# Optimization experiments

Hardware: AMD Instinct MI355X
Metric: run time of the kernel (lower is better)

Reference implementation:

```python
import jax, jax.numpy as jnp
import numpy as np

B, N, L = 256, 4096, 6
EMBED, HID, VOCAB = 16, 32, 200
NOTE, LSTM_D, T = 64, 64, 128


def _tree_structure():
    """One random tree of N nodes (root=node 0), tiled across the batch.
    height = distance above deepest descendant; children have strictly smaller height."""
    rng = np.random.default_rng(0)
    height = np.zeros(N, np.int32)
    height[0] = L
    height[1:] = rng.integers(0, L, N - 1)
    kind = np.full(N, 2, np.int32)  # 2 = internal
    leaf_mask = height == 0
    kind[leaf_mask] = (rng.random(leaf_mask.sum()) < 0.1).astype(np.int32)  # 1=ptr, 0=leaf
    parent = np.zeros(N, np.int64)
    for hl in range(L):
        mask = height == hl
        cand = np.where((height > hl) & (kind == 2))[0]  # root always qualifies
        parent[mask] = rng.choice(cand, size=int(mask.sum()))
    parent[0] = 0  # root points to itself; harmless (its own h stays 0 until final level)
    return height, kind, parent


def setup_inputs():
    height, kind, parent = _tree_structure()
    offs = (np.arange(B, dtype=np.int64) * N)[:, None]
    rng = np.random.default_rng(1)
    inp = {
        'kind': jnp.asarray(np.tile(kind, B), jnp.int32),
        'height': jnp.asarray(np.tile(height, B), jnp.int32),
        'parent': jnp.asarray((parent[None, :] + offs).reshape(-1), jnp.int32),
        'tok_a': jnp.asarray(rng.integers(0, VOCAB, B * N), jnp.int32),
        'tok_b': jnp.asarray(rng.integers(0, VOCAB, B * N), jnp.int32),
        'ptr_time': jnp.asarray(rng.integers(0, T, B * N), jnp.int32),
    }
    key = jax.random.key(0)
    ks = jax.random.split(key, 16)
    def w(k, shape, scale=0.05):
        return (jax.random.normal(k, shape, jnp.float32) * scale)
    inp['first_notes'] = w(ks[0], (B, NOTE), 1.0)
    inp['lstm_out'] = w(ks[1], (B, T, LSTM_D), 1.0)
    inp['embedding'] = w(ks[2], (VOCAB, EMBED), 0.02)
    inp['leaf_w1'] = w(ks[3], (2 * EMBED, HID)); inp['leaf_b1'] = w(ks[4], (HID,))
    inp['leaf_w2'] = w(ks[5], (HID, HID));       inp['leaf_b2'] = w(ks[6], (HID,))
    inp['node_w'] = w(ks[7], (2 * EMBED + HID, HID)); inp['node_b'] = w(ks[8], (HID,))
    inp['ptr_w'] = w(ks[9], (NOTE + LSTM_D, HID));    inp['ptr_b'] = w(ks[10], (HID,))
    inp['ff_w1'] = w(ks[11], (HID, HID)); inp['ff_b1'] = w(ks[12], (HID,))
    inp['ff_w2'] = w(ks[13], (HID, HID)); inp['ff_b2'] = w(ks[14], (HID,))
    inp['tail_w'] = w(ks[15], (HID, 1)); inp['tail_b'] = jnp.zeros((1,), jnp.float32)
    return inp


def reference(kind, height, parent, tok_a, tok_b, ptr_time, first_notes, lstm_out,
              embedding, leaf_w1, leaf_b1, leaf_w2, leaf_b2, node_w, node_b,
              ptr_w, ptr_b, ff_w1, ff_b1, ff_w2, ff_b2, tail_w, tail_b):
    M = kind.shape[0]
    nb = first_notes.shape[0]
    n_per = M // nb
    tree_id = jnp.arange(M, dtype=jnp.int32) // n_per
    emb_a = embedding[tok_a]  # [M, EMBED] (parent-type / first-token embed)
    emb_b = embedding[tok_b]  # [M, EMBED] (node-type / second-token embed)
    pair = jnp.concatenate([emb_a, emb_b], axis=-1)  # [M, 2*EMBED]
    # leaf path: two stacked linears (no nonlinearity), as in leaf_ff
    leaf_h = (pair @ leaf_w1 + leaf_b1) @ leaf_w2 + leaf_b2
    # ptr path: Linear(note_dim + lstm_out_dim -> hidden)
    ptr_in = jnp.concatenate([first_notes[tree_id], lstm_out[tree_id, ptr_time]], axis=-1)
    ptr_h = ptr_in @ ptr_w + ptr_b
    h = jnp.where((kind == 0)[:, None], leaf_h,
                  jnp.where((kind == 1)[:, None], ptr_h, 0.0))
    # level-synchronous child-sum: children always have smaller height
    for lvl in range(1, L + 1):
        csum = jax.ops.segment_sum(h, parent, num_segments=M)  # [M, HID]
        inner = jax.nn.relu(jnp.concatenate([pair, csum], axis=-1) @ node_w + node_b)
        h = jnp.where((height == lvl)[:, None], inner, h)
    roots = h[::n_per]  # [B, HID], root is node 0 of each tree block
    ff = (roots @ ff_w1 + ff_b1) @ ff_w2 + ff_b2
    return ff @ tail_w + tail_b  # [B, 1]


if __name__ == '__main__':
    out = reference(**setup_inputs())
    print(out.shape, out.dtype)
```

## Files before the change

### kernel.cpp

```cpp
#include <hip/hip_runtime.h>

#define BATCH   256
#define N_PER   4096
#define EMBED   16
#define HID     32
#define NOTE    64
#define LSTM_D  64
#define T_LEN   128
#define VOCAB   200
#define HSTR    (BATCH * HID)

#define MH_C0    0
#define MH_C1    1
#define MH_CNT   2
#define MH_P     7
#define MH_PBASE 8
#define OFF_K0N   64
#define OFF_K0S   (OFF_K0N + N_PER)
#define OFF_K1N   (OFF_K0S + N_PER)
#define OFF_K1S   (OFF_K1N + N_PER)
#define OFF_PLIST (OFF_K1S + N_PER)
#define OFF_WSLOT (OFF_PLIST + N_PER)
#define OFF_COFF  (OFF_WSLOT + N_PER)
#define EAW_OFF     (1024 * 1024)
#define EBW_OFF     (EAW_OFF + VOCAB * HID * 4)
#define FN_PRE_OFF  (1536 * 1024)
#define ROOTSUM_OFF (1792 * 1024)
#define PTRPRE_OFF  (2ull * 1024 * 1024)
#define H_OFF       (8ull * 1024 * 1024)

#define RCHUNK 16

__global__ __launch_bounds__(1024) void build_structure(
    const int* __restrict__ kind, const int* __restrict__ height,
    const int* __restrict__ parent, int* __restrict__ meta)
{
    __shared__ unsigned long long p64[1024];
    __shared__ int pint[1024];
    __shared__ int node2pidx[N_PER];
    __shared__ int deg[N_PER];
    __shared__ int sbases[8];
    __shared__ int stot[8];

    int t  = threadIdx.x;
    int i0 = 4 * t;

    int myb[4];
    #pragma unroll
    for (int q = 0; q < 4; ++q) {
        int i = i0 + q;
        int hgt = height[i];
        int b;
        if (hgt > 0) { b = 1 + hgt; if (b > 7) b = 7; }
        else b = (kind[i] == 0) ? 0 : 1;
        myb[q] = b;
    }
    unsigned long long clo = 0, chi = 0;
    #pragma unroll
    for (int q = 0; q < 4; ++q) {
        int b = myb[q];
        if (b < 4) clo += 1ull << (16 * b);
        else       chi += 1ull << (16 * (b - 4));
    }
    p64[t] = clo; __syncthreads();
    for (int off = 1; off < 1024; off <<= 1) {
        unsigned long long v = (t >= off) ? p64[t - off] : 0ull; __syncthreads();
        p64[t] += v; __syncthreads();
    }
    unsigned long long inc_lo = p64[t];
    if (t == 1023) {
        stot[0] = (int)(inc_lo & 0xFFFF);         stot[1] = (int)((inc_lo >> 16) & 0xFFFF);
        stot[2] = (int)((inc_lo >> 32) & 0xFFFF); stot[3] = (int)((inc_lo >> 48) & 0xFFFF);
    }
    __syncthreads();
    p64[t] = chi; __syncthreads();
    for (int off = 1; off < 1024; off <<= 1) {
        unsigned long long v = (t >= off) ? p64[t - off] : 0ull; __syncthreads();
        p64[t] += v; __syncthreads();
    }
    unsigned long long inc_hi = p64[t];
    if (t == 1023) {
        stot[4] = (int)(inc_hi & 0xFFFF);         stot[5] = (int)((inc_hi >> 16) & 0xFFFF);
        stot[6] = (int)((inc_hi >> 32) & 0xFFFF); stot[7] = (int)((inc_hi >> 48) & 0xFFFF);
    }
    __syncthreads();
    if (t == 0) {
        int s = 0;
        for (int b = 0; b < 8; ++b) { sbases[b] = s; s += stot[b]; }
        meta[MH_C0] = stot[0];
        meta[MH_C1] = stot[1];
        for (int l = 0; l < 5; ++l) meta[MH_CNT + l]   = stot[2 + l];
        for (int l = 0; l < 5; ++l) meta[MH_PBASE + l] = sbases[2 + l] - sbases[2];
        meta[MH_P] = (sbases[7] - sbases[2]) + stot[7];
    }
    __syncthreads();

    unsigned long long exlo = inc_lo - clo, exhi = inc_hi - chi;
    int mypos[4], mypidx[4];
    #pragma unroll
    for (int q = 0; q < 4; ++q) {
        int i = i0 + q, b = myb[q];
        int pos;
        if (b < 4) { pos = (int)((exlo >> (16 * b)) & 0xFFFF); exlo += 1ull << (16 * b); }
        else       { pos = (int)((exhi >> (16 * (b - 4))) & 0xFFFF); exhi += 1ull << (16 * (b - 4)); }
        mypos[q] = pos;
        int pidx = -1;
        if (b == 0)      meta[OFF_K0N + pos] = i;
        else if (b == 1) meta[OFF_K1N + pos] = i;
        else {
            pidx = (sbases[b] - sbases[2]) + pos;
            meta[OFF_PLIST + pidx] = i;
            node2pidx[i] = pidx;
        }
        mypidx[q] = pidx;
    }
    #pragma unroll
    for (int q = 0; q < 4; ++q) deg[i0 + q] = 0;
    __syncthreads();

    int par[4];
    #pragma unroll
    for (int q = 0; q < 4; ++q) {
        int i = i0 + q; par[q] = parent[i];
        if (i != 0) atomicAdd(&deg[node2pidx[par[q]]], 1);
    }
    __syncthreads();

    int d0 = deg[i0], d1 = deg[i0 + 1], d2 = deg[i0 + 2], d3 = deg[i0 + 3];
    int s4 = d0 + d1 + d2 + d3;
    pint[t] = s4; __syncthreads();
    for (int off = 1; off < 1024; off <<= 1) {
        int v = (t >= off) ? pint[t - off] : 0; __syncthreads();
        pint[t] += v; __syncthreads();
    }
    int ex = pint[t] - s4;
    int o0 = ex, o1 = ex + d0, o2 = o1 + d1, o3 = o2 + d2;
    deg[i0] = o0; deg[i0 + 1] = o1; deg[i0 + 2] = o2; deg[i0 + 3] = o3;
    meta[OFF_COFF + i0]     = o0;
    meta[OFF_COFF + i0 + 1] = o1;
    meta[OFF_COFF + i0 + 2] = o2;
    meta[OFF_COFF + i0 + 3] = o3;
    if (t == 1023) meta[OFF_COFF + N_PER] = o3 + d3;
    __syncthreads();

    #pragma unroll
    for (int q = 0; q < 4; ++q) {
        int i = i0 + q; if (i == 0) continue;
        int slot = atomicAdd(&deg[node2pidx[par[q]]], 1);
        int b = myb[q];
        if (b == 0)      meta[OFF_K0S + mypos[q]] = slot;
        else if (b == 1) meta[OFF_K1S + mypos[q]] = slot;
        else             meta[OFF_WSLOT + mypidx[q]] = slot;
    }
}

__global__ __launch_bounds__(256) void prep_kernel(
    const int* __restrict__ meta,
    const int* __restrict__ tok_a, const int* __restrict__ tok_b,
    const float* __restrict__ first_notes, const float* __restrict__ lstm_out,
    const float* __restrict__ embedding,
    const float* __restrict__ leaf_w1, const float* __restrict__ leaf_b1,
    const float* __restrict__ leaf_w2, const float* __restrict__ leaf_b2,
    const float* __restrict__ node_w,
    const float* __restrict__ ptr_w, const float* __restrict__ ptr_b,
    float* __restrict__ eaw_g, float* __restrict__ ebw_g,
    float* __restrict__ fn_pre, float* __restrict__ ptr_pre,
    float* __restrict__ h)
{
    int tid  = blockIdx.x * blockDim.x + threadIdx.x;
    int nthr = gridDim.x * blockDim.x;
    int lane = threadIdx.x & 31;
    int gid  = tid >> 5;
    int ngr  = nthr >> 5;

    for (int idx = tid; idx < VOCAB * HID; idx += nthr) {
        int v = idx >> 5, d = idx & 31;
        float sa = 0.f, sb = 0.f;
        #pragma unroll
        for (int k = 0; k < EMBED; ++k) {
            float e = embedding[v * EMBED + k];
            sa += e * node_w[k * HID + d];
            sb += e * node_w[(EMBED + k) * HID + d];
        }
        eaw_g[idx] = sa;
        ebw_g[idx] = sb;
    }

    for (int r = gid; r < BATCH; r += ngr) {
        const float* fn = first_notes + (size_t)r * NOTE;
        float v = ptr_b[lane];
        #pragma unroll
        for (int k = 0; k < NOTE; ++k) v += fn[k] * ptr_w[k * HID + lane];
        fn_pre[r * HID + lane] = v;
    }

    for (int r = gid; r < BATCH * T_LEN; r += ngr) {
        const float* lo = lstm_out + (size_t)r * LSTM_D;
        float v = 0.f;
        #pragma unroll
        for (int k = 0; k < LSTM_D; ++k) v += lo[k] * ptr_w[(NOTE + k) * HID + lane];
        ptr_pre[r * HID + lane] = v;
    }

    {
        int c0 = meta[MH_C0];
        const int* K0N = meta + OFF_K0N;
        const int* K0S = meta + OFF_K0S;
        float w1a[EMBED], w1b[EMBED], w2c[HID];
        #pragma unroll
        for (int k = 0; k < EMBED; ++k) {
            w1a[k] = leaf_w1[k * HID + lane];
            w1b[k] = leaf_w1[(EMBED + k) * HID + lane];
        }
        #pragma unroll
        for (int k = 0; k < HID; ++k) w2c[k] = leaf_w2[k * HID + lane];
        float b1 = leaf_b1[lane], b2 = leaf_b2[lane];

        int tot = c0 * BATCH;
        for (int i = gid; i < tot; i += ngr) {
            int j = i >> 8, tree = i & 255;
            int node = K0N[j], slot = K0S[j];
            int gn = tree * N_PER + node;
            const float* ea = embedding + tok_a[gn] * EMBED;
            const float* eb = embedding + tok_b[gn] * EMBED;
            float hid = b1;
            #pragma unroll
            for (int k = 0; k < EMBED; ++k) hid += ea[k] * w1a[k];
            #pragma unroll
            for (int k = 0; k < EMBED; ++k) hid += eb[k] * w1b[k];
            float v = b2;
            #pragma unroll
            for (int k = 0; k < HID; ++k) v += __shfl(hid, k, 32) * w2c[k];
            h[(size_t)slot * HSTR + tree * HID + lane] = v;
        }
    }
}

__global__ __launch_bounds__(256) void ptr_kernel(
    const int* __restrict__ meta, const int* __restrict__ ptr_time,
    const float* __restrict__ fn_pre, const float* __restrict__ ptr_pre,
    float* __restrict__ h)
{
    int c1 = meta[MH_C1];
    const int* K1N = meta + OFF_K1N;
    const int* K1S = meta + OFF_K1S;
    int lane = threadIdx.x & 31;
    int gid  = (blockIdx.x * blockDim.x + threadIdx.x) >> 5;
    int ngr  = (gridDim.x * blockDim.x) >> 5;

    int tot = c1 * BATCH;
    for (int i = gid; i < tot; i += ngr) {
        int j = i >> 8, tree = i & 255;
        int node = K1N[j], slot = K1S[j];
        int tt = ptr_time[tree * N_PER + node];
        float v = fn_pre[tree * HID + lane]
                + ptr_pre[((size_t)tree * T_LEN + tt) * HID + lane];
        h[(size_t)slot * HSTR + tree * HID + lane] = v;
    }
}

__global__ __launch_bounds__(256) void level_kernel(
    const int* __restrict__ meta,
    const int* __restrict__ tok_a, const int* __restrict__ tok_b,
    const float* __restrict__ eaw_g, const float* __restrict__ ebw_g,
    const float* __restrict__ node_w, const float* __restrict__ node_b,
    float* __restrict__ h, int lvl)
{
    int cnt = meta[MH_CNT + lvl];
    int pb  = meta[MH_PBASE + lvl];
    const int* PL = meta + OFF_PLIST;
    const int* WS = meta + OFF_WSLOT;
    const int* CO = meta + OFF_COFF;

    int lane = threadIdx.x & 31;
    int gid  = (blockIdx.x * blockDim.x + threadIdx.x) >> 5;
    int ngr  = (gridDim.x * blockDim.x) >> 5;

    float wc[HID];
    #pragma unroll
    for (int k = 0; k < HID; ++k) wc[k] = node_w[(2 * EMBED + k) * HID + lane];
    float nb = node_b[lane];

    int perchunk = cnt << 5;
    int tot = cnt * BATCH;
    for (int i = gid; i < tot; i += ngr) {
        int tchunk = i / perchunk;
        int r      = i - tchunk * perchunk;
        int rr     = r >> 5;
        int tree   = (tchunk << 5) + (r & 31);
        int pidx = pb + rr;
        int node = PL[pidx], wslot = WS[pidx];
        int e = CO[pidx], e1 = CO[pidx + 1];

        const float* hb = h + (size_t)tree * HID + lane;
        float csum = 0.f;
        for (int c = e; c < e1; ++c) csum += hb[(size_t)c * HSTR];

        int gn = tree * N_PER + node;
        int ta = tok_a[gn], tb = tok_b[gn];
        float v = nb + eaw_g[ta * HID + lane] + ebw_g[tb * HID + lane];
        #pragma unroll
        for (int k = 0; k < HID; ++k) v += __shfl(csum, k, 32) * wc[k];
        v = fmaxf(v, 0.f);
        h[(size_t)wslot * HSTR + tree * HID + lane] = v;
    }
}

__global__ __launch_bounds__(256) void root_gather_kernel(
    const int* __restrict__ meta, const float* __restrict__ h,
    float* __restrict__ rootsum)
{
    const int* CO = meta + OFF_COFF;
    int P = meta[MH_P];
    int e = CO[P - 1], e1 = CO[P];
    int n = e1 - e;
    int per = (n + RCHUNK - 1) / RCHUNK;

    int t = blockIdx.x * blockDim.x + threadIdx.x;
    int lane  = t & 31;
    int tree  = (t >> 5) & 255;
    int chunk = t >> 13;
    if (chunk >= RCHUNK) return;

    int s  = e + chunk * per;
    int en = s + per; if (en > e1) en = e1;
    if (s >= en) return;
    float sum = 0.f;
    for (int c = s; c < en; ++c)
        sum += h[(size_t)c * HSTR + tree * HID + lane];
    atomicAdd(&rootsum[tree * HID + lane], sum);
}

__global__ __launch_bounds__(256) void final_kernel(
    const int* __restrict__ meta,
    const int* __restrict__ tok_a, const int* __restrict__ tok_b,
    const float* __restrict__ eaw_g, const float* __restrict__ ebw_g,
    const float* __restrict__ rootsum,
    const float* __restrict__ node_w, const float* __restrict__ node_b,
    const float* __restrict__ ff_w1, const float* __restrict__ ff_b1,
    const float* __restrict__ ff_w2, const float* __restrict__ ff_b2,
    const float* __restrict__ tail_w, const float* __restrict__ tail_b,
    float* __restrict__ out)
{
    int tree = (blockIdx.x * blockDim.x + threadIdx.x) >> 5;
    int lane = threadIdx.x & 31;
    if (tree >= BATCH) return;

    float csum = rootsum[tree * HID + lane];
    int gn = tree * N_PER;
    int ta = tok_a[gn], tb = tok_b[gn];
    float v = node_b[lane] + eaw_g[ta * HID + lane] + ebw_g[tb * HID + lane];
    #pragma unroll
    for (int k = 0; k < HID; ++k)
        v += __shfl(csum, k, 32) * node_w[(2 * EMBED + k) * HID + lane];
    v = fmaxf(v, 0.f);

    float f1 = ff_b1[lane];
    #pragma unroll
    for (int k = 0; k < HID; ++k) f1 += __shfl(v, k, 32) * ff_w1[k * HID + lane];
    float f2 = ff_b2[lane];
    #pragma unroll
    for (int k = 0; k < HID; ++k) f2 += __shfl(f1, k, 32) * ff_w2[k * HID + lane];

    float c2 = f2 * tail_w[lane];
    #pragma unroll
    for (int off = 16; off > 0; off >>= 1) c2 += __shfl_down(c2, off, 32);
    if (lane == 0) out[tree] = c2 + tail_b[0];
}

extern "C" void kernel_launch(void* const* d_in, const int* in_sizes, int n_in,
                              void* d_out, int out_size, void* d_ws, size_t ws_size,
                              hipStream_t stream) {
    const int*   kind        = (const int*)d_in[0];
    const int*   height      = (const int*)d_in[1];
    const int*   parent      = (const int*)d_in[2];
    const int*   tok_a       = (const int*)d_in[3];
    const int*   tok_b       = (const int*)d_in[4];
    const int*   ptr_time    = (const int*)d_in[5];
    const float* first_notes = (const float*)d_in[6];
    const float* lstm_out    = (const float*)d_in[7];
    const float* embedding   = (const float*)d_in[8];
    const float* leaf_w1     = (const float*)d_in[9];
    const float* leaf_b1     = (const float*)d_in[10];
    const float* leaf_w2     = (const float*)d_in[11];
    const float* leaf_b2     = (const float*)d_in[12];
    const float* node_w      = (const float*)d_in[13];
    const float* node_b      = (const float*)d_in[14];
    const float* ptr_w       = (const float*)d_in[15];
    const float* ptr_b       = (const float*)d_in[16];
    const float* ff_w1       = (const float*)d_in[17];
    const float* ff_b1       = (const float*)d_in[18];
    const float* ff_w2       = (const float*)d_in[19];
    const float* ff_b2       = (const float*)d_in[20];
    const float* tail_w      = (const float*)d_in[21];
    const float* tail_b      = (const float*)d_in[22];

    char* ws = (char*)d_ws;
    int*   meta    = (int*)ws;
    float* eaw_g   = (float*)(ws + EAW_OFF);
    float* ebw_g   = (float*)(ws + EBW_OFF);
    float* fn_pre  = (float*)(ws + FN_PRE_OFF);
    float* rootsum = (float*)(ws + ROOTSUM_OFF);
    float* ptr_pre = (float*)(ws + PTRPRE_OFF);
    float* h       = (float*)(ws + H_OFF);

    hipMemsetAsync(rootsum, 0, BATCH * HID * sizeof(float), stream);

    build_structure<<<1, 1024, 0, stream>>>(kind, height, parent, meta);

    prep_kernel<<<2048, 256, 0, stream>>>(
        meta, tok_a, tok_b, first_notes, lstm_out, embedding,
        leaf_w1, leaf_b1, leaf_w2, leaf_b2, node_w, ptr_w, ptr_b,
        eaw_g, ebw_g, fn_pre, ptr_pre, h);

    ptr_kernel<<<2048, 256, 0, stream>>>(meta, ptr_time, fn_pre, ptr_pre, h);

    for (int lvl = 0; lvl < 5; ++lvl) {
        level_kernel<<<4096, 256, 0, stream>>>(
            meta, tok_a, tok_b, eaw_g, ebw_g, node_w, node_b, h, lvl);
    }

    root_gather_kernel<<<(RCHUNK * BATCH * HID) / 256, 256, 0, stream>>>(
        meta, h, rootsum);

    final_kernel<<<32, 256, 0, stream>>>(
        meta, tok_a, tok_b, eaw_g, ebw_g, rootsum, node_w, node_b,
        ff_w1, ff_b1, ff_w2, ff_b2, tail_w, tail_b, (float*)d_out);
}
```

Before: 399.6 us.

## Fold leaf MLP into vocab tables, compute ptr rows on demand, use wave scans

The structure builder now uses wavefront shuffle scans instead of block-wide shared-memory scans. It also precomputes per-vocab leaf tables (embedding·W1·W2) and the node_w embedding projections, so leaf nodes become two table lookups plus a constant. The ptr path no longer precomputes projections for all B·T lstm rows; it computes only the needed ptr nodes directly, which removes the separate ptr kernel and a large intermediate buffer. The level kernel child-sum is unrolled four ways with independent accumulators. The trade-offs are a redundant ptr_w dot product per ptr node and extra serial work in the single-block build kernel.

Result: slower. 433.6 us (+8.5%).

```diff
diff --git a/kernel.cpp b/kernel.cpp
--- a/kernel.cpp
+++ b/kernel.cpp
@@ -24,19 +24,34 @@
 #define OFF_COFF  (OFF_WSLOT + N_PER)
 #define EAW_OFF     (1024 * 1024)
 #define EBW_OFF     (EAW_OFF + VOCAB * HID * 4)
-#define FN_PRE_OFF  (1536 * 1024)
+#define LA2_OFF     (EBW_OFF + VOCAB * HID * 4)
+#define LB2_OFF     (LA2_OFF + VOCAB * HID * 4)
+#define CC_OFF      (LB2_OFF + VOCAB * HID * 4)
 #define ROOTSUM_OFF (1792 * 1024)
-#define PTRPRE_OFF  (2ull * 1024 * 1024)
 #define H_OFF       (8ull * 1024 * 1024)
 
 #define RCHUNK 16
+
+__device__ __forceinline__ unsigned long long shflup64(unsigned long long x, int off) {
+    unsigned lo = (unsigned)(x & 0xffffffffull);
+    unsigned hi = (unsigned)(x >> 32);
+    lo = __shfl_up(lo, off, 64);
+    hi = __shfl_up(hi, off, 64);
+    return ((unsigned long long)hi << 32) | (unsigned long long)lo;
+}
 
 __global__ __launch_bounds__(1024) void build_structure(
     const int* __restrict__ kind, const int* __restrict__ height,
-    const int* __restrict__ parent, int* __restrict__ meta)
+    const int* __restrict__ parent, int* __restrict__ meta,
+    const float* __restrict__ embedding,
+    const float* __restrict__ leaf_w1, const float* __restrict__ leaf_b1,
+    const float* __restrict__ leaf_w2, const float* __restrict__ leaf_b2,
+    const float* __restrict__ node_w,
+    float* __restrict__ eaw_g, float* __restrict__ ebw_g,
+    float* __restrict__ la2, float* __restrict__ lb2, float* __restrict__ cc)
 {
-    __shared__ unsigned long long p64[1024];
-    __shared__ int pint[1024];
+    __shared__ unsigned long long wlo[16], whi[16];
+    __shared__ int wint[16];
     __shared__ int node2pidx[N_PER];
     __shared__ int deg[N_PER];
     __shared__ int sbases[8];
@@ -44,6 +59,8 @@
 
     int t  = threadIdx.x;
     int i0 = 4 * t;
+    int laneid = t & 63;
+    int wid    = t >> 6;
 
     int myb[4];
     #pragma unroll
@@ -62,31 +79,28 @@
         if (b < 4) clo += 1ull << (16 * b);
         else       chi += 1ull << (16 * (b - 4));
     }
-    p64[t] = clo; __syncthreads();
-    for (int off = 1; off < 1024; off <<= 1) {
-        unsigned long long v = (t >= off) ? p64[t - off] : 0ull; __syncthreads();
-        p64[t] += v; __syncthreads();
-    }
-    unsigned long long inc_lo = p64[t];
-    if (t == 1023) {
-        stot[0] = (int)(inc_lo & 0xFFFF);         stot[1] = (int)((inc_lo >> 16) & 0xFFFF);
-        stot[2] = (int)((inc_lo >> 32) & 0xFFFF); stot[3] = (int)((inc_lo >> 48) & 0xFFFF);
-    }
-    __syncthreads();
-    p64[t] = chi; __syncthreads();
-    for (int off = 1; off < 1024; off <<= 1) {
-        unsigned long long v = (t >= off) ? p64[t - off] : 0ull; __syncthreads();
-        p64[t] += v; __syncthreads();
-    }
-    unsigned long long inc_hi = p64[t];
-    if (t == 1023) {
-        stot[4] = (int)(inc_hi & 0xFFFF);         stot[5] = (int)((inc_hi >> 16) & 0xFFFF);
-        stot[6] = (int)((inc_hi >> 32) & 0xFFFF); stot[7] = (int)((inc_hi >> 48) & 0xFFFF);
-    }
-    __syncthreads();
+
+    unsigned long long a = clo, b64 = chi;
+    #pragma unroll
+    for (int off = 1; off < 64; off <<= 1) {
+        unsigned long long ua = shflup64(a, off);
+        unsigned long long ub = shflup64(b64, off);
+        if (laneid >= off) { a += ua; b64 += ub; }
+    }
+    if (laneid == 63) { wlo[wid] = a; whi[wid] = b64; }
+    __syncthreads();
+    unsigned long long blo = 0, bhi = 0;
+    for (int w = 0; w < wid; ++w) { blo += wlo[w]; bhi += whi[w]; }
+    unsigned long long inc_lo = a + blo, inc_hi = b64 + bhi;
     if (t == 0) {
+        unsigned long long tlo = 0, thi = 0;
+        for (int w = 0; w < 16; ++w) { tlo += wlo[w]; thi += whi[w]; }
+        stot[0] = (int)(tlo & 0xFFFF);         stot[1] = (int)((tlo >> 16) & 0xFFFF);
+        stot[2] = (int)((tlo >> 32) & 0xFFFF); stot[3] = (int)((tlo >> 48) & 0xFFFF);
+        stot[4] = (int)(thi & 0xFFFF);         stot[5] = (int)((thi >> 16) & 0xFFFF);
+        stot[6] = (int)((thi >> 32) & 0xFFFF); stot[7] = (int)((thi >> 48) & 0xFFFF);
         int s = 0;
-        for (int b = 0; b < 8; ++b) { sbases[b] = s; s += stot[b]; }
+        for (int bb = 0; bb < 8; ++bb) { sbases[bb] = s; s += stot[bb]; }
         meta[MH_C0] = stot[0];
         meta[MH_C1] = stot[1];
         for (int l = 0; l < 5; ++l) meta[MH_CNT + l]   = stot[2 + l];
@@ -128,12 +142,20 @@
 
     int d0 = deg[i0], d1 = deg[i0 + 1], d2 = deg[i0 + 2], d3 = deg[i0 + 3];
     int s4 = d0 + d1 + d2 + d3;
-    pint[t] = s4; __syncthreads();
-    for (int off = 1; off < 1024; off <<= 1) {
-        int v = (t >= off) ? pint[t - off] : 0; __syncthreads();
-        pint[t] += v; __syncthreads();
-    }
-    int ex = pint[t] - s4;
+
+    int vi = s4;
+    #pragma unroll
+    for (int off = 1; off < 64; off <<= 1) {
+        int u = __shfl_up(vi, off, 64);
+        if (laneid >= off) vi += u;
+    }
+    if (laneid == 63) wint[wid] = vi;
+    __syncthreads();
+    int bint = 0;
+    for (int w = 0; w < wid; ++w) bint += wint[w];
+    int incl = vi + bint;
+
+    int ex = incl - s4;
     int o0 = ex, o1 = ex + d0, o2 = o1 + d1, o3 = o2 + d2;
     deg[i0] = o0; deg[i0 + 1] = o1; deg[i0 + 2] = o2; deg[i0 + 3] = o3;
     meta[OFF_COFF + i0]     = o0;
@@ -152,19 +174,49 @@
         else if (b == 1) meta[OFF_K1S + mypos[q]] = slot;
         else             meta[OFF_WSLOT + mypidx[q]] = slot;
     }
+
+    {
+        int hw = t >> 5, ln = t & 31;
+        for (int v = hw; v < VOCAB; v += 32) {
+            const float* ev = embedding + v * EMBED;
+            float ea = 0.f, eb = 0.f, t1a = 0.f, t1b = 0.f;
+            #pragma unroll
+            for (int k = 0; k < EMBED; ++k) {
+                float e = ev[k];
+                ea  += e * node_w[k * HID + ln];
+                eb  += e * node_w[(EMBED + k) * HID + ln];
+                t1a += e * leaf_w1[k * HID + ln];
+                t1b += e * leaf_w1[(EMBED + k) * HID + ln];
+            }
+            eaw_g[v * HID + ln] = ea;
+            ebw_g[v * HID + ln] = eb;
+            float a2 = 0.f, b2v = 0.f;
+            #pragma unroll
+            for (int k = 0; k < HID; ++k) {
+                float w2 = leaf_w2[k * HID + ln];
+                a2  += __shfl(t1a, k, 32) * w2;
+                b2v += __shfl(t1b, k, 32) * w2;
+            }
+            la2[v * HID + ln] = a2;
+            lb2[v * HID + ln] = b2v;
+        }
+        if (t < HID) {
+            float c = leaf_b2[t];
+            #pragma unroll
+            for (int k = 0; k < HID; ++k) c += leaf_b1[k] * leaf_w2[k * HID + t];
+            cc[t] = c;
+        }
+    }
 }
 
 __global__ __launch_bounds__(256) void prep_kernel(
     const int* __restrict__ meta,
     const int* __restrict__ tok_a, const int* __restrict__ tok_b,
+    const int* __restrict__ ptr_time,
     const float* __restrict__ first_notes, const float* __restrict__ lstm_out,
-    const float* __restrict__ embedding,
-    const float* __restrict__ leaf_w1, const float* __restrict__ leaf_b1,
-    const float* __restrict__ leaf_w2, const float* __restrict__ leaf_b2,
-    const float* __restrict__ node_w,
+    const float* __restrict__ la2, const float* __restrict__ lb2,
+    const float* __restrict__ cc,
     const float* __restrict__ ptr_w, const float* __restrict__ ptr_b,
-    float* __restrict__ eaw_g, float* __restrict__ ebw_g,
-    float* __restrict__ fn_pre, float* __restrict__ ptr_pre,
     float* __restrict__ h)
 {
     int tid  = blockIdx.x * blockDim.x + threadIdx.x;
@@ -173,89 +225,42 @@
     int gid  = tid >> 5;
     int ngr  = nthr >> 5;
 
-    for (int idx = tid; idx < VOCAB * HID; idx += nthr) {
-        int v = idx >> 5, d = idx & 31;
-        float sa = 0.f, sb = 0.f;
-        #pragma unroll
-        for (int k = 0; k < EMBED; ++k) {
-            float e = embedding[v * EMBED + k];
-            sa += e * node_w[k * HID + d];
-            sb += e * node_w[(EMBED + k) * HID + d];
-        }
-        eaw_g[idx] = sa;
-        ebw_g[idx] = sb;
-    }
-
-    for (int r = gid; r < BATCH; r += ngr) {
-        const float* fn = first_notes + (size_t)r * NOTE;
-        float v = ptr_b[lane];
-        #pragma unroll
-        for (int k = 0; k < NOTE; ++k) v += fn[k] * ptr_w[k * HID + lane];
-        fn_pre[r * HID + lane] = v;
-    }
-
-    for (int r = gid; r < BATCH * T_LEN; r += ngr) {
-        const float* lo = lstm_out + (size_t)r * LSTM_D;
-        float v = 0.f;
-        #pragma unroll
-        for (int k = 0; k < LSTM_D; ++k) v += lo[k] * ptr_w[(NOTE + k) * HID + lane];
-        ptr_pre[r * HID + lane] = v;
-    }
-
     {
+        float ccv = cc[lane];
         int c0 = meta[MH_C0];
         const int* K0N = meta + OFF_K0N;
         const int* K0S = meta + OFF_K0S;
-        float w1a[EMBED], w1b[EMBED], w2c[HID];
-        #pragma unroll
-        for (int k = 0; k < EMBED; ++k) {
-            w1a[k] = leaf_w1[k * HID + lane];
-            w1b[k] = leaf_w1[(EMBED + k) * HID + lane];
-        }
-        #pragma unroll
-        for (int k = 0; k < HID; ++k) w2c[k] = leaf_w2[k * HID + lane];
-        float b1 = leaf_b1[lane], b2 = leaf_b2[lane];
-
         int tot = c0 * BATCH;
         for (int i = gid; i < tot; i += ngr) {
             int j = i >> 8, tree = i & 255;
             int node = K0N[j], slot = K0S[j];
             int gn = tree * N_PER + node;
-            const float* ea = embedding + tok_a[gn] * EMBED;
-            const float* eb = embedding + tok_b[gn] * EMBED;
-            float hid = b1;
+            int ta = tok_a[gn], tb = tok_b[gn];
+            h[(size_t)slot * HSTR + tree * HID + lane] =
+                ccv + la2[ta * HID + lane] + lb2[tb * HID + lane];
+        }
+    }
+
+    {
+        float pb = ptr_b[lane];
+        int c1 = meta[MH_C1];
+        const int* K1N = meta + OFF_K1N;
+        const int* K1S = meta + OFF_K1S;
+        int tot = c1 * BATCH;
+        for (int i = gid; i < tot; i += ngr) {
+            int j = i >> 8, tree = i & 255;
+            int node = K1N[j], slot = K1S[j];
+            int gn = tree * N_PER + node;
+            int tt = ptr_time[gn];
+            const float* fn = first_notes + (size_t)tree * NOTE;
+            const float* lo = lstm_out + ((size_t)tree * T_LEN + tt) * LSTM_D;
+            float v = pb;
             #pragma unroll
-            for (int k = 0; k < EMBED; ++k) hid += ea[k] * w1a[k];
+            for (int k = 0; k < NOTE; ++k)   v += fn[k] * ptr_w[k * HID + lane];
             #pragma unroll
-            for (int k = 0; k < EMBED; ++k) hid += eb[k] * w1b[k];
-            float v = b2;
-            #pragma unroll
-            for (int k = 0; k < HID; ++k) v += __shfl(hid, k, 32) * w2c[k];
+            for (int k = 0; k < LSTM_D; ++k) v += lo[k] * ptr_w[(NOTE + k) * HID + lane];
             h[(size_t)slot * HSTR + tree * HID + lane] = v;
         }
-    }
-}
-
-__global__ __launch_bounds__(256) void ptr_kernel(
-    const int* __restrict__ meta, const int* __restrict__ ptr_time,
-    const float* __restrict__ fn_pre, const float* __restrict__ ptr_pre,
-    float* __restrict__ h)
-{
-    int c1 = meta[MH_C1];
-    const int* K1N = meta + OFF_K1N;
-    const int* K1S = meta + OFF_K1S;
-    int lane = threadIdx.x & 31;
-    int gid  = (blockIdx.x * blockDim.x + threadIdx.x) >> 5;
-    int ngr  = (gridDim.x * blockDim.x) >> 5;
-
-    int tot = c1 * BATCH;
-    for (int i = gid; i < tot; i += ngr) {
-        int j = i >> 8, tree = i & 255;
-        int node = K1N[j], slot = K1S[j];
-        int tt = ptr_time[tree * N_PER + node];
-        float v = fn_pre[tree * HID + lane]
-                + ptr_pre[((size_t)tree * T_LEN + tt) * HID + lane];
-        h[(size_t)slot * HSTR + tree * HID + lane] = v;
     }
 }
 
@@ -293,8 +298,16 @@
         int e = CO[pidx], e1 = CO[pidx + 1];
 
         const float* hb = h + (size_t)tree * HID + lane;
-        float csum = 0.f;
-        for (int c = e; c < e1; ++c) csum += hb[(size_t)c * HSTR];
+        float s0 = 0.f, s1 = 0.f, s2 = 0.f, s3 = 0.f;
+        int c = e;
+        for (; c + 4 <= e1; c += 4) {
+            s0 += hb[(size_t)(c)     * HSTR];
+            s1 += hb[(size_t)(c + 1) * HSTR];
+            s2 += hb[(size_t)(c + 2) * HSTR];
+            s3 += hb[(size_t)(c + 3) * HSTR];
+        }
+        for (; c < e1; ++c) s0 += hb[(size_t)c * HSTR];
+        float csum = (s0 + s1) + (s2 + s3);
 
         int gn = tree * N_PER + node;
         int ta = tok_a[gn], tb = tok_b[gn];
@@ -399,21 +412,22 @@
     int*   meta    = (int*)ws;
     float* eaw_g   = (float*)(ws + EAW_OFF);
     float* ebw_g   = (float*)(ws + EBW_OFF);
-    float* fn_pre  = (float*)(ws + FN_PRE_OFF);
+    float* la2     = (float*)(ws + LA2_OFF);
+    float* lb2     = (float*)(ws + LB2_OFF);
+    float* cc      = (float*)(ws + CC_OFF);
     float* rootsum = (float*)(ws + ROOTSUM_OFF);
-    float* ptr_pre = (float*)(ws + PTRPRE_OFF);
     float* h       = (float*)(ws + H_OFF);
 
     hipMemsetAsync(rootsum, 0, BATCH * HID * sizeof(float), stream);
 
-    build_structure<<<1, 1024, 0, stream>>>(kind, height, parent, meta);
+    build_structure<<<1, 1024, 0, stream>>>(
+        kind, height, parent, meta,
+        embedding, leaf_w1, leaf_b1, leaf_w2, leaf_b2, node_w,
+        eaw_g, ebw_g, la2, lb2, cc);
 
     prep_kernel<<<2048, 256, 0, stream>>>(
-        meta, tok_a, tok_b, first_notes, lstm_out, embedding,
-        leaf_w1, leaf_b1, leaf_w2, leaf_b2, node_w, ptr_w, ptr_b,
-        eaw_g, ebw_g, fn_pre, ptr_pre, h);
-
-    ptr_kernel<<<2048, 256, 0, stream>>>(meta, ptr_time, fn_pre, ptr_pre, h);
+        meta, tok_a, tok_b, ptr_time, first_notes, lstm_out,
+        la2, lb2, cc, ptr_w, ptr_b, h);
 
     for (int lvl = 0; lvl < 5; ++lvl) {
         level_kernel<<<4096, 256, 0, stream>>>(
```
